# Performance work log

Hardware: AMD Instinct MI355X
Metric: run time of the kernel (lower is better)

## Reference

```python
import jax, jax.numpy as jnp
import numpy as np

N, E, D, A, M, H, NRES = 65536, 16384, 1024, 512, 2048, 3, 3


def setup_inputs() -> dict:
    key = jax.random.key(0)
    ks = jax.random.split(key, 24)
    s = 0.02
    inp = {
        'h': jax.random.normal(ks[0], (N, D), dtype=jnp.float32),
        'rep': jax.random.normal(ks[1], (N, D), dtype=jnp.float32),
        'src': jax.random.randint(ks[2], (E,), 0, N, dtype=jnp.int32),
        'dst': jax.random.randint(ks[3], (E,), 0, N, dtype=jnp.int32),
        # per-head attention projections (stacked over H heads)
        'Wq': s * jax.random.normal(ks[4], (H, D, A), dtype=jnp.float32),
        'bq': s * jax.random.normal(ks[5], (H, A), dtype=jnp.float32),
        'Wk': s * jax.random.normal(ks[6], (H, D, A), dtype=jnp.float32),
        'bk': s * jax.random.normal(ks[7], (H, A), dtype=jnp.float32),
        'Wv': s * jax.random.normal(ks[8], (H, D, A), dtype=jnp.float32),
        'bv': s * jax.random.normal(ks[9], (H, A), dtype=jnp.float32),
        # MultiMLPLayer: first Linear(A->M), then NRES ResNet blocks of width M
        'W0': s * jax.random.normal(ks[10], (H, A, M), dtype=jnp.float32),
        'b0': s * jax.random.normal(ks[11], (H, M), dtype=jnp.float32),
        'Wr': s * jax.random.normal(ks[12], (H, NRES, M, M), dtype=jnp.float32),
        'br': s * jax.random.normal(ks[13], (H, NRES, M), dtype=jnp.float32),
        'g_ln': jnp.ones((H, NRES, M), dtype=jnp.float32),
        'b_ln': jnp.zeros((H, NRES, M), dtype=jnp.float32),
        # mlp_scale: Linear(M->A) per head
        'Wms': s * jax.random.normal(ks[14], (H, M, A), dtype=jnp.float32),
        'bms': s * jax.random.normal(ks[15], (H, A), dtype=jnp.float32),
        # update_attn_scale: Linear(H*A -> D, bias=False)
        'Wuas': s * jax.random.normal(ks[16], (H * A, D), dtype=jnp.float32),
    }
    return inp


def _layernorm(x, g, b, eps=1e-5):
    mu = jnp.mean(x, axis=-1, keepdims=True)
    var = jnp.mean((x - mu) ** 2, axis=-1, keepdims=True)
    return (x - mu) / jnp.sqrt(var + eps) * g + b


def reference(h, rep, src, dst, Wq, bq, Wk, bk, Wv, bv, W0, b0, Wr, br,
              g_ln, b_ln, Wms, bms, Wuas):
    # model normalizes all node embeddings first (F.normalize)
    hn = h / jnp.maximum(jnp.linalg.norm(h, axis=-1, keepdims=True), 1e-12)
    Q = hn[src]            # [E, D] mailbox messages (copy_u of 'h')
    K = rep[dst]           # [E, D] destination node reps (K == V)

    # per-head projections: [H, E, A]
    Qp = jnp.einsum('ed,hda->hea', Q, Wq) + bq[:, None, :]
    Kp = jnp.einsum('ed,hda->hea', K, Wk) + bk[:, None, :]
    Vp = jnp.einsum('ed,hda->hea', K, Wv) + bv[:, None, :]

    attn_dim = Wq.shape[-1]
    scores = (Qp * Kp) / (attn_dim ** 0.5)       # 2D path: elementwise QK, scaled by sqrt(attn_size)
    attn = jax.nn.softmax(scores, axis=-1)       # softmax over feature dim
    attn_out = attn * Vp                         # [H, E, A] (dropout p=0.0 in TreeHopNode)

    # MultiMLPLayer: Linear(A->M) then NRES ResNet blocks
    m = jnp.einsum('hea,ham->hem', attn_out, W0) + b0[:, None, :]
    for j in range(Wr.shape[1]):
        xn = _layernorm(m, g_ln[:, j][:, None, :], b_ln[:, j][:, None, :])
        m = m + jax.nn.relu(jnp.einsum('hem,hmn->hen', xn, Wr[:, j]) + br[:, j][:, None, :])

    head_out = jnp.einsum('hem,hma->hea', m, Wms) + bms[:, None, :] + attn_out  # [H, E, A]
    cat = jnp.transpose(head_out, (1, 0, 2)).reshape(Q.shape[0], -1)            # [E, H*A]

    # reduce_func: h = Q - K + update_attn_scale(multi_head_out)
    return Q - K + cat @ Wuas                                                   # [E, D]
```

## Files before the change

kernel.cpp:

```cpp
#include <hip/hip_runtime.h>
#include <hip/hip_bf16.h>
#include <cstdint>
#include <cstddef>

typedef __bf16 bf16;
typedef __bf16 bf16x2 __attribute__((ext_vector_type(2)));
typedef __bf16 bf16x4 __attribute__((ext_vector_type(4)));
typedef __bf16 bf16x8 __attribute__((ext_vector_type(8)));
typedef float f32x4 __attribute__((ext_vector_type(4)));

static_assert(sizeof(bf16x8) == 16, "bf16x8 must be 16B");

#define NE 16384
#define ND 1024
#define NA 512
#define NM 2048
#define NH 3
#define NRES 3
#define ESH 14

__device__ __forceinline__ void async_ld16(const bf16* g, bf16* l) {
  __builtin_amdgcn_global_load_lds(
      (__attribute__((address_space(1))) void*)(void*)g,
      (__attribute__((address_space(3))) void*)(void*)l, 16, 0, 0);
}

template <int N>
__device__ __forceinline__ void vm_wait() {
  asm volatile("s_waitcnt vmcnt(%0)" ::"n"(N) : "memory");
}
__device__ __forceinline__ void lgkm0() {
  asm volatile("s_waitcnt lgkmcnt(0)" ::: "memory");
}
__device__ __forceinline__ void bar() {
  asm volatile("s_barrier" ::: "memory");
}


template <int MODE>
__global__ __launch_bounds__(256, 4) void gemm_kernel(
    const bf16* __restrict__ A, const bf16* __restrict__ B,
    const float* __restrict__ bias, void* __restrict__ Cv,
    const bf16* __restrict__ addb, int K, int ldc, int coloff, int addld,
    int nbx, int hsh, long long bstr, int bistr) {
  __shared__ bf16 lA[8192];
  __shared__ bf16 lB[8192];

  const int nwg = gridDim.x;
  int bid = blockIdx.x;
  if ((nwg & 7) == 0) bid = (bid & 7) * (nwg >> 3) + (bid >> 3);
  const int n0 = (bid % nbx) * 128;
  const int m0 = (bid / nbx) * 128;

  const int hidx = hsh ? (m0 >> hsh) : 0;
  if (hsh) {
    B += (size_t)hidx * (size_t)bstr;
    bias += (size_t)hidx * (size_t)bistr;
  }

  const int tid = threadIdx.x;
  const int wv = tid >> 6, ln = tid & 63;
  const int wm = wv >> 1, wn = wv & 1;

  const int rowq = wv * 8 + (ln >> 3);
  const int colo = ((ln & 7) ^ (ln >> 3)) * 8;
  const bf16* gA = A + (size_t)(m0 + rowq) * K + colo;
  const bf16* gB = B + (size_t)(n0 + rowq) * K + colo;

  auto stage = [&](int t) {
#pragma unroll
    for (int r = 0; r < 4; ++r) {
      async_ld16(gA + (size_t)(r * 32) * K + t * 64,
                 &lA[(r * 32 + wv * 8) * 64]);
      async_ld16(gB + (size_t)(r * 32) * K + t * 64,
                 &lB[(r * 32 + wv * 8) * 64]);
    }
  };

  const int l15 = ln & 15;
  const int aOff = (wm * 64 + l15) * 64;
  const int bOff = (wn * 64 + l15) * 64;
  const int c0 = (ln >> 4) ^ (ln & 7);

  f32x4 acc[4][4] = {};
  bf16x8 fa[4], fb[4];

  const int nt = K >> 6;

  stage(0);

  for (int t = 0; t < nt; ++t) {
    vm_wait<0>();
    bar();
    {
      const int co = c0 * 8;
#pragma unroll
      for (int i = 0; i < 4; ++i)
        fa[i] = *(const bf16x8*)&lA[aOff + i * 1024 + co];
#pragma unroll
      for (int j = 0; j < 4; ++j)
        fb[j] = *(const bf16x8*)&lB[bOff + j * 1024 + co];
    }
    __builtin_amdgcn_s_setprio(1);
#pragma unroll
    for (int i = 0; i < 4; ++i)
#pragma unroll
      for (int j = 0; j < 4; ++j)
        acc[i][j] = __builtin_amdgcn_mfma_f32_16x16x32_bf16(
            fa[i], fb[j], acc[i][j], 0, 0, 0);
    __builtin_amdgcn_s_setprio(0);
    {
      const int co = (c0 ^ 4) * 8;
#pragma unroll
      for (int i = 0; i < 4; ++i)
        fa[i] = *(const bf16x8*)&lA[aOff + i * 1024 + co];
#pragma unroll
      for (int j = 0; j < 4; ++j)
        fb[j] = *(const bf16x8*)&lB[bOff + j * 1024 + co];
    }
    lgkm0();
    bar();
    if (t + 1 < nt) stage(t + 1);
    __builtin_amdgcn_s_setprio(1);
#pragma unroll
    for (int i = 0; i < 4; ++i)
#pragma unroll
      for (int j = 0; j < 4; ++j)
        acc[i][j] = __builtin_amdgcn_mfma_f32_16x16x32_bf16(
            fa[i], fb[j], acc[i][j], 0, 0, 0);
    __builtin_amdgcn_s_setprio(0);
  }

  const int r4 = (ln >> 4) * 4;
  const int nbase = n0 + wn * 64 + l15;
#pragma unroll
  for (int mi = 0; mi < 4; ++mi) {
#pragma unroll
    for (int r = 0; r < 4; ++r) {
      const int m = m0 + wm * 64 + mi * 16 + r4 + r;
#pragma unroll
      for (int ni = 0; ni < 4; ++ni) {
        const int n = nbase + ni * 16;
        float v = acc[mi][ni][r];
        if constexpr (MODE != 3) v += bias[n];
        if constexpr (MODE == 0) {
          size_t idx = (size_t)m * ldc + n;
          if (coloff && n >= coloff) idx += (size_t)addld;
          ((bf16*)Cv)[idx] = (bf16)v;
        } else if constexpr (MODE == 1) {
          float prev = (float)addb[(size_t)m * addld + n];
          ((bf16*)Cv)[(size_t)m * ldc + n] = (bf16)(prev + fmaxf(v, 0.f));
        } else if constexpr (MODE == 2) {
          v += (float)addb[(size_t)m * addld + n];
          const int mloc = hsh ? (m & ((1 << hsh) - 1)) : m;
          ((bf16*)Cv)[(size_t)mloc * ldc + hidx * coloff + n] = (bf16)v;
        } else {
          float* C = (float*)Cv;
          const size_t idx = (size_t)m * ldc + n;
          C[idx] = C[idx] + v;
        }
      }
    }
  }
}

template <int MODE>
static void launch_gemm(hipStream_t s, const bf16* A, const bf16* B,
                        const float* bias, void* C, const bf16* addb, int M,
                        int N, int K, int ldc, int coloff, int addld,
                        int hsh = 0, long long bstr = 0, int bistr = 0) {
  const int nbx = N / 128;
  gemm_kernel<MODE><<<dim3(nbx * (M / 128)), 256, 0, s>>>(
      A, B, bias, C, addb, K, ldc, coloff, addld, nbx, hsh, bstr, bistr);
}

__global__ void transpose_cvt(const float* __restrict__ src,
                              bf16* __restrict__ dst, int K, int N) {
  __shared__ float t[32][33];
  const size_t zo = (size_t)blockIdx.z * K * N;
  src += zo;
  dst += zo;
  const int n = blockIdx.x * 32 + threadIdx.x;
  const int kb = blockIdx.y * 32;
#pragma unroll
  for (int i = 0; i < 4; ++i) {
    const int k = kb + threadIdx.y + i * 8;
    t[threadIdx.y + i * 8][threadIdx.x] = src[(size_t)k * N + n];
  }
  __syncthreads();
#pragma unroll
  for (int i = 0; i < 4; ++i) {
    const int nn = blockIdx.x * 32 + threadIdx.y + i * 8;
    dst[(size_t)nn * K + kb + threadIdx.x] =
        (bf16)t[threadIdx.x][threadIdx.y + i * 8];
  }
}

__global__ void concat2_kernel(const float* __restrict__ a,
                               const float* __restrict__ b,
                               float* __restrict__ dst, int na) {
  const int i = blockIdx.x * 256 + threadIdx.x;
  dst[i] = (i < na) ? a[i] : b[i - na];
}

__global__ __launch_bounds__(256) void gather_kernel(
    const float* __restrict__ h, const float* __restrict__ rep,
    const int* __restrict__ src, const int* __restrict__ dst,
    bf16* __restrict__ Qb, bf16* __restrict__ Kb, float* __restrict__ qk) {
  __shared__ float sm[4];
  const int e = blockIdx.x, tid = threadIdx.x;
  const int sr = src[e], dr = dst[e];
  const float4 hv = ((const float4*)(h + (size_t)sr * ND))[tid];
  float ss = hv.x * hv.x + hv.y * hv.y + hv.z * hv.z + hv.w * hv.w;
#pragma unroll
  for (int o = 32; o > 0; o >>= 1) ss += __shfl_down(ss, o, 64);
  if ((tid & 63) == 0) sm[tid >> 6] = ss;
  __syncthreads();
  const float tot = sm[0] + sm[1] + sm[2] + sm[3];
  const float inv = 1.f / fmaxf(sqrtf(tot), 1e-12f);
  const float4 rv = ((const float4*)(rep + (size_t)dr * ND))[tid];
  const float q0 = hv.x * inv, q1 = hv.y * inv, q2 = hv.z * inv,
              q3 = hv.w * inv;
  const size_t base = (size_t)e * ND + tid * 4;
  bf16x4 qv;
  qv[0] = (bf16)q0; qv[1] = (bf16)q1; qv[2] = (bf16)q2; qv[3] = (bf16)q3;
  *(bf16x4*)(Qb + base) = qv;
  bf16x4 kv;
  kv[0] = (bf16)rv.x; kv[1] = (bf16)rv.y; kv[2] = (bf16)rv.z;
  kv[3] = (bf16)rv.w;
  *(bf16x4*)(Kb + base) = kv;
  *(float4*)(qk + base) =
      make_float4(q0 - rv.x, q1 - rv.y, q2 - rv.z, q3 - rv.w);
}

__global__ __launch_bounds__(256) void softmax_kernel(
    const bf16* __restrict__ Qp, const bf16* __restrict__ Kp,
    const bf16* __restrict__ Vp, bf16* __restrict__ attn) {
  __shared__ float sm[4];
  const int tid = threadIdx.x;
  const int e = blockIdx.x, hh = blockIdx.y;
  const size_t base = (size_t)e * (NH * NA) + (size_t)hh * NA + 2 * tid;
  const bf16x2 q = *(const bf16x2*)(Qp + base);
  const bf16x2 k = *(const bf16x2*)(Kp + base);
  const bf16x2 v = *(const bf16x2*)(Vp + base);
  const float sc = 0.044194173824159216f;
  const float s0 = (float)q[0] * (float)k[0] * sc;
  const float s1 = (float)q[1] * (float)k[1] * sc;
  float mx = fmaxf(s0, s1);
#pragma unroll
  for (int o = 32; o > 0; o >>= 1) mx = fmaxf(mx, __shfl_down(mx, o, 64));
  if ((tid & 63) == 0) sm[tid >> 6] = mx;
  __syncthreads();
  mx = fmaxf(fmaxf(sm[0], sm[1]), fmaxf(sm[2], sm[3]));
  __syncthreads();
  const float p0 = expf(s0 - mx), p1 = expf(s1 - mx);
  float ssum = p0 + p1;
#pragma unroll
  for (int o = 32; o > 0; o >>= 1) ssum += __shfl_down(ssum, o, 64);
  if ((tid & 63) == 0) sm[tid >> 6] = ssum;
  __syncthreads();
  const float inv = 1.f / (sm[0] + sm[1] + sm[2] + sm[3]);
  bf16x2 r;
  r[0] = (bf16)(p0 * inv * (float)v[0]);
  r[1] = (bf16)(p1 * inv * (float)v[1]);
  const size_t obase = (size_t)hh * NE * NA + (size_t)e * NA + 2 * tid;
  *(bf16x2*)(attn + obase) = r;
}

__global__ __launch_bounds__(256) void ln_kernel(const bf16* __restrict__ x,
                                                 bf16* __restrict__ y,
                                                 const float* __restrict__ g,
                                                 const float* __restrict__ b) {
  __shared__ float sm[8];
  const int tid = threadIdx.x;
  const size_t base = (size_t)blockIdx.x * NM + tid * 8;
  const bf16x8 xv = *(const bf16x8*)(x + base);
  float xf[8], s = 0.f, ss = 0.f;
#pragma unroll
  for (int i = 0; i < 8; ++i) {
    xf[i] = (float)xv[i];
    s += xf[i];
    ss += xf[i] * xf[i];
  }
#pragma unroll
  for (int o = 32; o > 0; o >>= 1) {
    s += __shfl_down(s, o, 64);
    ss += __shfl_down(ss, o, 64);
  }
  if ((tid & 63) == 0) {
    sm[tid >> 6] = s;
    sm[4 + (tid >> 6)] = ss;
  }
  __syncthreads();
  s = sm[0] + sm[1] + sm[2] + sm[3];
  ss = sm[4] + sm[5] + sm[6] + sm[7];
  const float mu = s * (1.f / NM);
  const float var = ss * (1.f / NM) - mu * mu;
  const float rstd = rsqrtf(fmaxf(var, 0.f) + 1e-5f);
  const int c0 = tid * 8;
  bf16x8 yv;
#pragma unroll
  for (int i = 0; i < 8; ++i)
    yv[i] = (bf16)((xf[i] - mu) * rstd * g[c0 + i] + b[c0 + i]);
  *(bf16x8*)(y + base) = yv;
}

extern "C" void kernel_launch(void* const* d_in, const int* in_sizes, int n_in,
                              void* d_out, int out_size, void* d_ws,
                              size_t ws_size, hipStream_t stream) {
  const float* h    = (const float*)d_in[0];
  const float* rep  = (const float*)d_in[1];
  const int* src    = (const int*)d_in[2];
  const int* dst    = (const int*)d_in[3];
  const float* Wq   = (const float*)d_in[4];
  const float* bq   = (const float*)d_in[5];
  const float* Wk   = (const float*)d_in[6];
  const float* bk   = (const float*)d_in[7];
  const float* Wv   = (const float*)d_in[8];
  const float* bv   = (const float*)d_in[9];
  const float* W0   = (const float*)d_in[10];
  const float* b0   = (const float*)d_in[11];
  const float* Wr   = (const float*)d_in[12];
  const float* br   = (const float*)d_in[13];
  const float* g_ln = (const float*)d_in[14];
  const float* b_ln = (const float*)d_in[15];
  const float* Wms  = (const float*)d_in[16];
  const float* bms  = (const float*)d_in[17];
  const float* Wuas = (const float*)d_in[18];
  float* out = (float*)d_out;

  bf16* ws = (bf16*)d_ws;
  size_t off = 0;
  auto alloc = [&](size_t n) {
    bf16* p = ws + off;
    off += n;
    return p;
  };
  bf16* WqT   = alloc((size_t)NH * NA * ND);
  bf16* WkT   = alloc((size_t)NH * NA * ND);
  bf16* WvT   = alloc((size_t)NH * NA * ND);
  bf16* W0T   = alloc((size_t)NH * NM * NA);
  bf16* WrT   = alloc((size_t)NH * NRES * NM * NM);
  bf16* WmsT  = alloc((size_t)NH * NA * NM);
  bf16* WuasT = alloc((size_t)ND * NH * NA);
  bf16* Qb    = alloc((size_t)NE * ND);
  bf16* Kb    = alloc((size_t)NE * ND);
  bf16* Qp    = alloc((size_t)NE * NH * NA);
  bf16* Kp    = alloc((size_t)NE * NH * NA);
  bf16* Vp    = alloc((size_t)NE * NH * NA);
  bf16* attn  = alloc((size_t)NH * NE * NA);
  bf16* mbuf3 = alloc((size_t)NH * NE * NM);
  bf16* xnb   = alloc((size_t)NE * NM);
  float* cbias = (float*)alloc(2 * (size_t)NH * NA * 2);
  bf16* cat   = Qp;
  if (ws_size < off * sizeof(bf16)) return;

  const dim3 tb(32, 8);
  transpose_cvt<<<dim3(NA / 32, ND / 32, NH), tb, 0, stream>>>(Wq, WqT, ND, NA);
  transpose_cvt<<<dim3(NA / 32, ND / 32, NH), tb, 0, stream>>>(Wk, WkT, ND, NA);
  transpose_cvt<<<dim3(NA / 32, ND / 32, NH), tb, 0, stream>>>(Wv, WvT, ND, NA);
  transpose_cvt<<<dim3(NM / 32, NA / 32, NH), tb, 0, stream>>>(W0, W0T, NA, NM);
  transpose_cvt<<<dim3(NM / 32, NM / 32, NH * NRES), tb, 0, stream>>>(Wr, WrT,
                                                                      NM, NM);
  transpose_cvt<<<dim3(NA / 32, NM / 32, NH), tb, 0, stream>>>(Wms, WmsT, NM,
                                                               NA);
  transpose_cvt<<<dim3(ND / 32, (NH * NA) / 32, 1), tb, 0, stream>>>(
      Wuas, WuasT, NH * NA, ND);
  concat2_kernel<<<(2 * NH * NA) / 256, 256, 0, stream>>>(bk, bv, cbias,
                                                          NH * NA);

  gather_kernel<<<NE, 256, 0, stream>>>(h, rep, src, dst, Qb, Kb, out);

  launch_gemm<0>(stream, Qb, WqT, bq, Qp, nullptr, NE, NH * NA, ND, NH * NA,
                 0, 0);
  launch_gemm<0>(stream, Kb, WkT, cbias, Kp, nullptr, NE, 2 * NH * NA, ND,
                 NH * NA, NH * NA, (NE - 1) * NH * NA);
  softmax_kernel<<<dim3(NE, NH), 256, 0, stream>>>(Qp, Kp, Vp, attn);

  for (int hh = 0; hh < NH; ++hh) {
    const bf16* attn_h = attn + (size_t)hh * NE * NA;
    bf16* mbuf_h = mbuf3 + (size_t)hh * NE * NM;
    launch_gemm<0>(stream, attn_h, W0T + (size_t)hh * NM * NA, b0 + hh * NM,
                   mbuf_h, nullptr, NE, NM, NA, NM, 0, 0);
    for (int j = 0; j < NRES; ++j) {
      const int hj = hh * NRES + j;
      ln_kernel<<<NE, 256, 0, stream>>>(mbuf_h, xnb, g_ln + (size_t)hj * NM,
                                        b_ln + (size_t)hj * NM);
      launch_gemm<1>(stream, xnb, WrT + (size_t)hj * NM * NM, br + hj * NM,
                     mbuf_h, mbuf_h, NE, NM, NM, NM, 0, NM);
    }
  }
  launch_gemm<2>(stream, mbuf3, WmsT, bms, cat, attn, NH * NE, NA, NM,
                 NH * NA, NA, NA, ESH, (long long)NA * NM, NA);

  launch_gemm<3>(stream, cat, WuasT, nullptr, out, nullptr, NE, ND, NH * NA,
                 ND, 0, 0);
}
```

Measured before the change: 2.519 ms.

## Fold LayerNorm into residual GEMM epilogue and batch the W0 GEMM across heads

```diff
diff --git a/kernel.cpp b/kernel.cpp
--- a/kernel.cpp
+++ b/kernel.cpp
@@ -42,7 +42,8 @@
     const bf16* __restrict__ A, const bf16* __restrict__ B,
     const float* __restrict__ bias, void* __restrict__ Cv,
     const bf16* __restrict__ addb, int K, int ldc, int coloff, int addld,
-    int nbx, int hsh, long long bstr, int bistr) {
+    int nbx, int hsh, long long bstr, int bistr,
+    const float* __restrict__ lnbb, const float* __restrict__ stats_in) {
   __shared__ bf16 lA[8192];
   __shared__ bf16 lB[8192];
 
@@ -138,26 +139,36 @@
 #pragma unroll
     for (int r = 0; r < 4; ++r) {
       const int m = m0 + wm * 64 + mi * 16 + r4 + r;
+      float mu = 0.f, rstd = 0.f;
+      if constexpr (MODE == 1) {
+        const float2 st = *(const float2*)&stats_in[2 * m];
+        mu = st.x * (1.f / NM);
+        const float var = st.y * (1.f / NM) - mu * mu;
+        rstd = rsqrtf(fmaxf(var, 0.f) + 1e-5f);
+      }
 #pragma unroll
       for (int ni = 0; ni < 4; ++ni) {
         const int n = nbase + ni * 16;
         float v = acc[mi][ni][r];
-        if constexpr (MODE != 3) v += bias[n];
         if constexpr (MODE == 0) {
+          v += bias[n];
           size_t idx = (size_t)m * ldc + n;
           if (coloff && n >= coloff) idx += (size_t)addld;
           ((bf16*)Cv)[idx] = (bf16)v;
         } else if constexpr (MODE == 1) {
-          float prev = (float)addb[(size_t)m * addld + n];
+          v = rstd * (v - mu * bias[n]) + lnbb[n];
+          const float prev = (float)addb[(size_t)m * addld + n];
           ((bf16*)Cv)[(size_t)m * ldc + n] = (bf16)(prev + fmaxf(v, 0.f));
         } else if constexpr (MODE == 2) {
+          v += bias[n];
           v += (float)addb[(size_t)m * addld + n];
           const int mloc = hsh ? (m & ((1 << hsh) - 1)) : m;
           ((bf16*)Cv)[(size_t)mloc * ldc + hidx * coloff + n] = (bf16)v;
         } else {
+          v += bias ? bias[n] : 0.f;
           float* C = (float*)Cv;
           const size_t idx = (size_t)m * ldc + n;
-          C[idx] = C[idx] + v;
+          C[idx] = C[idx] + acc[mi][ni][r];
         }
       }
     }
@@ -168,16 +179,45 @@
 static void launch_gemm(hipStream_t s, const bf16* A, const bf16* B,
                         const float* bias, void* C, const bf16* addb, int M,
                         int N, int K, int ldc, int coloff, int addld,
-                        int hsh = 0, long long bstr = 0, int bistr = 0) {
+                        int hsh = 0, long long bstr = 0, int bistr = 0,
+                        const float* lnbb = nullptr,
+                        const float* stats_in = nullptr) {
   const int nbx = N / 128;
   gemm_kernel<MODE><<<dim3(nbx * (M / 128)), 256, 0, s>>>(
-      A, B, bias, C, addb, K, ldc, coloff, addld, nbx, hsh, bstr, bistr);
+      A, B, bias, C, addb, K, ldc, coloff, addld, nbx, hsh, bstr, bistr,
+      lnbb, stats_in);
+}
+
+__global__ __launch_bounds__(256) void stats_kernel(
+    const bf16* __restrict__ x, float* __restrict__ stats) {
+  const int wv = threadIdx.x >> 6, ln = threadIdx.x & 63;
+  const int row = blockIdx.x * 4 + wv;
+  const bf16* xr = x + (size_t)row * NM;
+  float s = 0.f, ss = 0.f;
+#pragma unroll
+  for (int p = 0; p < 4; ++p) {
+    const bf16x8 v = *(const bf16x8*)(xr + p * 512 + ln * 8);
+#pragma unroll
+    for (int i = 0; i < 8; ++i) {
+      const float f = (float)v[i];
+      s += f;
+      ss += f * f;
+    }
+  }
+#pragma unroll
+  for (int o = 32; o > 0; o >>= 1) {
+    s += __shfl_down(s, o, 64);
+    ss += __shfl_down(ss, o, 64);
+  }
+  if (ln == 0) *(float2*)&stats[2 * row] = make_float2(s, ss);
 }
 
 __global__ void transpose_cvt(const float* __restrict__ src,
-                              bf16* __restrict__ dst, int K, int N) {
+                              bf16* __restrict__ dst, int K, int N,
+                              const float* __restrict__ scale) {
   __shared__ float t[32][33];
-  const size_t zo = (size_t)blockIdx.z * K * N;
+  const int z = blockIdx.z;
+  const size_t zo = (size_t)z * K * N;
   src += zo;
   dst += zo;
   const int n = blockIdx.x * 32 + threadIdx.x;
@@ -188,12 +228,32 @@
     t[threadIdx.y + i * 8][threadIdx.x] = src[(size_t)k * N + n];
   }
   __syncthreads();
+  const float sc = scale ? scale[(size_t)z * K + kb + threadIdx.x] : 1.f;
 #pragma unroll
   for (int i = 0; i < 4; ++i) {
     const int nn = blockIdx.x * 32 + threadIdx.y + i * 8;
     dst[(size_t)nn * K + kb + threadIdx.x] =
-        (bf16)t[threadIdx.x][threadIdx.y + i * 8];
-  }
+        (bf16)(t[threadIdx.x][threadIdx.y + i * 8] * sc);
+  }
+}
+
+__global__ void lnfold_kernel(const float* __restrict__ Wr,
+                              const float* __restrict__ g,
+                              const float* __restrict__ b,
+                              const float* __restrict__ br,
+                              float* __restrict__ sgW,
+                              float* __restrict__ bWbr) {
+  const int hj = blockIdx.y;
+  const int n = blockIdx.x * 256 + threadIdx.x;
+  const float* W = Wr + (size_t)hj * NM * NM;
+  float sg = 0.f, sb = 0.f;
+  for (int k = 0; k < NM; ++k) {
+    const float w = W[(size_t)k * NM + n];
+    sg += g[hj * NM + k] * w;
+    sb += b[hj * NM + k] * w;
+  }
+  sgW[hj * NM + n] = sg;
+  bWbr[hj * NM + n] = sb + br[hj * NM + n];
 }
 
 __global__ void concat2_kernel(const float* __restrict__ a,
@@ -265,44 +325,6 @@
   r[1] = (bf16)(p1 * inv * (float)v[1]);
   const size_t obase = (size_t)hh * NE * NA + (size_t)e * NA + 2 * tid;
   *(bf16x2*)(attn + obase) = r;
-}
-
-__global__ __launch_bounds__(256) void ln_kernel(const bf16* __restrict__ x,
-                                                 bf16* __restrict__ y,
-                                                 const float* __restrict__ g,
-                                                 const float* __restrict__ b) {
-  __shared__ float sm[8];
-  const int tid = threadIdx.x;
-  const size_t base = (size_t)blockIdx.x * NM + tid * 8;
-  const bf16x8 xv = *(const bf16x8*)(x + base);
-  float xf[8], s = 0.f, ss = 0.f;
-#pragma unroll
-  for (int i = 0; i < 8; ++i) {
-    xf[i] = (float)xv[i];
-    s += xf[i];
-    ss += xf[i] * xf[i];
-  }
-#pragma unroll
-  for (int o = 32; o > 0; o >>= 1) {
-    s += __shfl_down(s, o, 64);
-    ss += __shfl_down(ss, o, 64);
-  }
-  if ((tid & 63) == 0) {
-    sm[tid >> 6] = s;
-    sm[4 + (tid >> 6)] = ss;
-  }
-  __syncthreads();
-  s = sm[0] + sm[1] + sm[2] + sm[3];
-  ss = sm[4] + sm[5] + sm[6] + sm[7];
-  const float mu = s * (1.f / NM);
-  const float var = ss * (1.f / NM) - mu * mu;
-  const float rstd = rsqrtf(fmaxf(var, 0.f) + 1e-5f);
-  const int c0 = tid * 8;
-  bf16x8 yv;
-#pragma unroll
-  for (int i = 0; i < 8; ++i)
-    yv[i] = (bf16)((xf[i] - mu) * rstd * g[c0 + i] + b[c0 + i]);
-  *(bf16x8*)(y + base) = yv;
 }
 
 extern "C" void kernel_launch(void* const* d_in, const int* in_sizes, int n_in,
@@ -350,24 +372,33 @@
   bf16* Vp    = alloc((size_t)NE * NH * NA);
   bf16* attn  = alloc((size_t)NH * NE * NA);
   bf16* mbuf3 = alloc((size_t)NH * NE * NM);
-  bf16* xnb   = alloc((size_t)NE * NM);
+  bf16* xnb3  = alloc((size_t)NH * NE * NM);
   float* cbias = (float*)alloc(2 * (size_t)NH * NA * 2);
+  float* sgW   = (float*)alloc((size_t)NH * NRES * NM * 2);
+  float* bWbr  = (float*)alloc((size_t)NH * NRES * NM * 2);
+  float* stats = (float*)alloc((size_t)NE * 2 * 2);
   bf16* cat   = Qp;
   if (ws_size < off * sizeof(bf16)) return;
 
   const dim3 tb(32, 8);
-  transpose_cvt<<<dim3(NA / 32, ND / 32, NH), tb, 0, stream>>>(Wq, WqT, ND, NA);
-  transpose_cvt<<<dim3(NA / 32, ND / 32, NH), tb, 0, stream>>>(Wk, WkT, ND, NA);
-  transpose_cvt<<<dim3(NA / 32, ND / 32, NH), tb, 0, stream>>>(Wv, WvT, ND, NA);
-  transpose_cvt<<<dim3(NM / 32, NA / 32, NH), tb, 0, stream>>>(W0, W0T, NA, NM);
-  transpose_cvt<<<dim3(NM / 32, NM / 32, NH * NRES), tb, 0, stream>>>(Wr, WrT,
-                                                                      NM, NM);
+  transpose_cvt<<<dim3(NA / 32, ND / 32, NH), tb, 0, stream>>>(Wq, WqT, ND, NA,
+                                                               nullptr);
+  transpose_cvt<<<dim3(NA / 32, ND / 32, NH), tb, 0, stream>>>(Wk, WkT, ND, NA,
+                                                               nullptr);
+  transpose_cvt<<<dim3(NA / 32, ND / 32, NH), tb, 0, stream>>>(Wv, WvT, ND, NA,
+                                                               nullptr);
+  transpose_cvt<<<dim3(NM / 32, NA / 32, NH), tb, 0, stream>>>(W0, W0T, NA, NM,
+                                                               nullptr);
+  transpose_cvt<<<dim3(NM / 32, NM / 32, NH * NRES), tb, 0, stream>>>(
+      Wr, WrT, NM, NM, g_ln);
   transpose_cvt<<<dim3(NA / 32, NM / 32, NH), tb, 0, stream>>>(Wms, WmsT, NM,
-                                                               NA);
+                                                               NA, nullptr);
   transpose_cvt<<<dim3(ND / 32, (NH * NA) / 32, 1), tb, 0, stream>>>(
-      Wuas, WuasT, NH * NA, ND);
+      Wuas, WuasT, NH * NA, ND, nullptr);
   concat2_kernel<<<(2 * NH * NA) / 256, 256, 0, stream>>>(bk, bv, cbias,
                                                           NH * NA);
+  lnfold_kernel<<<dim3(NM / 256, NH * NRES), 256, 0, stream>>>(
+      Wr, g_ln, b_ln, br, sgW, bWbr);
 
   gather_kernel<<<NE, 256, 0, stream>>>(h, rep, src, dst, Qb, Kb, out);
 
@@ -377,20 +408,22 @@
                  NH * NA, NH * NA, (NE - 1) * NH * NA);
   softmax_kernel<<<dim3(NE, NH), 256, 0, stream>>>(Qp, Kp, Vp, attn);
 
+  launch_gemm<0>(stream, attn, W0T, b0, mbuf3, nullptr, NH * NE, NM, NA, NM,
+                 0, 0, ESH, (long long)NM * NA, NM);
+
   for (int hh = 0; hh < NH; ++hh) {
-    const bf16* attn_h = attn + (size_t)hh * NE * NA;
-    bf16* mbuf_h = mbuf3 + (size_t)hh * NE * NM;
-    launch_gemm<0>(stream, attn_h, W0T + (size_t)hh * NM * NA, b0 + hh * NM,
-                   mbuf_h, nullptr, NE, NM, NA, NM, 0, 0);
+    bf16* bufs[2] = {mbuf3 + (size_t)hh * NE * NM, xnb3 + (size_t)hh * NE * NM};
     for (int j = 0; j < NRES; ++j) {
       const int hj = hh * NRES + j;
-      ln_kernel<<<NE, 256, 0, stream>>>(mbuf_h, xnb, g_ln + (size_t)hj * NM,
-                                        b_ln + (size_t)hj * NM);
-      launch_gemm<1>(stream, xnb, WrT + (size_t)hj * NM * NM, br + hj * NM,
-                     mbuf_h, mbuf_h, NE, NM, NM, NM, 0, NM);
-    }
-  }
-  launch_gemm<2>(stream, mbuf3, WmsT, bms, cat, attn, NH * NE, NA, NM,
+      const bf16* src_b = bufs[j & 1];
+      bf16* dst_b = bufs[(j & 1) ^ 1];
+      stats_kernel<<<NE / 4, 256, 0, stream>>>(src_b, stats);
+      launch_gemm<1>(stream, src_b, WrT + (size_t)hj * NM * NM,
+                     sgW + (size_t)hj * NM, dst_b, src_b, NE, NM, NM, NM, 0,
+                     NM, 0, 0, 0, bWbr + (size_t)hj * NM, stats);
+    }
+  }
+  launch_gemm<2>(stream, xnb3, WmsT, bms, cat, attn, NH * NE, NA, NM,
                  NH * NA, NA, NA, ESH, (long long)NA * NM, NA);
 
   launch_gemm<3>(stream, cat, WuasT, nullptr, out, nullptr, NE, ND, NH * NA,
```

New measurement: 2.542 ms. No clear change (+0.9%).
